# Kernel optimization log

Measured on AMD Instinct MI355X. Metric: run time of the kernel, lower is better.

The kernel has to match this reference:

```python
import jax, jax.numpy as jnp
import numpy as np

POS_W = 1.0
ANG_W = 1.0
WID_W = 1.0
N = 1048560  # predictions (divisible by 17)
M = 8388480  # total GT grasps = sum(arange(N) % 17)


def setup_inputs() -> dict:
    key = jax.random.key(0)
    k1, k2 = jax.random.split(key)
    pred = jax.random.normal(k1, (N, 6), dtype=jnp.float32)
    all_targets = jax.random.normal(k2, (M, 6), dtype=jnp.float32)
    # ragged counts in [0, 16]; sum == M exactly
    target_counts = (jnp.arange(N, dtype=jnp.int64) % 17)
    return {"pred": pred, "all_targets": all_targets, "target_counts": target_counts}


def _smooth_l1(x):
    a = jnp.abs(x)
    return jnp.where(a < 1.0, 0.5 * x * x, a - 0.5)


def reference(pred, all_targets, target_counts):
    n = pred.shape[0]
    m = all_targets.shape[0]
    # segment id for each GT row (contiguous slices, order of target_counts)
    seg = jnp.repeat(jnp.arange(n), target_counts, total_repeat_length=m)  # (M,)
    p = pred[seg]  # (M,6) gathered predictions
    dp = p[:, :2] - all_targets[:, :2]
    da = p[:, 2:4] - all_targets[:, 2:4]
    dw = p[:, 4] - all_targets[:, 4]
    dist = (POS_W * jnp.sum(dp * dp, axis=-1)
            + ANG_W * jnp.sum(da * da, axis=-1)
            + WID_W * dw * dw)  # (M,)
    # ragged argmin per segment (first occurrence, like torch.argmin)
    min_d = jax.ops.segment_min(dist, seg, num_segments=n)  # (N,)
    row = jnp.arange(m)
    cand = jnp.where(dist == min_d[seg], row, m)
    arg = jax.ops.segment_min(cand, seg, num_segments=n)  # (N,) global row idx or m
    has = target_counts > 0
    gt = all_targets[jnp.where(has, jnp.clip(arg, 0, m - 1), 0)]  # (N,6)
    # fused per-prediction loss against the closest GT
    loss_pos = jnp.sum(_smooth_l1(pred[:, :2] - gt[:, :2]), axis=-1)
    loss_ang = jnp.sum(jnp.abs(pred[:, 2:4] - gt[:, 2:4]), axis=-1)
    loss_wid = _smooth_l1(pred[:, 4] - gt[:, 4])
    losses = jnp.where(has, POS_W * loss_pos + ANG_W * loss_ang + WID_W * loss_wid, 0.0)
    return jnp.mean(losses)  # reduction='mean'
```

## Files before the change

### kernel.cpp

```cpp
#include <hip/hip_runtime.h>
#include <math.h>

#define POS_W 1.0f
#define ANG_W 1.0f
#define WID_W 1.0f
#define CHUNK 1024
#define F2PT 12

__device__ __forceinline__ float smooth_l1(float x) {
    float a = fabsf(x);
    return a < 1.0f ? 0.5f * x * x : a - 0.5f;
}

__global__ void k_block_sums(const int* __restrict__ counts, int stride, int n,
                             int* __restrict__ blockSums) {
    int i = blockIdx.x * 256 + threadIdx.x;
    int c = (i < n) ? counts[(long long)i * stride] : 0;
    for (int off = 32; off > 0; off >>= 1) c += __shfl_down(c, off, 64);
    __shared__ int sdata[4];
    int lane = threadIdx.x & 63, wave = threadIdx.x >> 6;
    if (lane == 0) sdata[wave] = c;
    __syncthreads();
    if (threadIdx.x == 0)
        blockSums[blockIdx.x] = sdata[0] + sdata[1] + sdata[2] + sdata[3];
}

__global__ __launch_bounds__(256) void k_loss(
    const float* __restrict__ pred, const float* __restrict__ tgt,
    const int* __restrict__ counts, int stride, int n,
    const int* __restrict__ blockSums, float invN, float* __restrict__ out) {
    __shared__ float2 ch[CHUNK * 3];
    __shared__ int wsum[4];
    __shared__ int wpre[4];
    __shared__ float fs[4];

    int t = threadIdx.x;
    int lane = t & 63, wave = t >> 6;
    int b = blockIdx.x;
    int i = b * 256 + t;
    int c = (i < n) ? counts[(long long)i * stride] : 0;

    int pre = 0;
    for (int j = t; j < b; j += 256) pre += blockSums[j];

    int incl = c;
#pragma unroll
    for (int d = 1; d < 64; d <<= 1) {
        int v = __shfl_up(incl, d, 64);
        if (lane >= d) incl += v;
    }
    for (int o = 32; o > 0; o >>= 1) pre += __shfl_down(pre, o, 64);
    if (lane == 63) wsum[wave] = incl;
    if (lane == 0) wpre[wave] = pre;

    bool active = (i < n) && (c > 0);
    float p0 = 0, p1 = 0, p2 = 0, p3 = 0, p4 = 0;
    if (active) {
        const float2* p2p = (const float2*)(pred + (long long)i * 6);
        float2 a = p2p[0], bb = p2p[1], w = p2p[2];
        p0 = a.x; p1 = a.y; p2 = bb.x; p3 = bb.y; p4 = w.x;
    }

    __syncthreads();
    int w0 = wsum[0], w1 = wsum[1], w2 = wsum[2], w3 = wsum[3];
    int waveOff = (wave > 0 ? w0 : 0) + (wave > 1 ? w1 : 0) + (wave > 2 ? w2 : 0);
    int off = waveOff + incl - c;
    int total = w0 + w1 + w2 + w3;
    int winStart = wpre[0] + wpre[1] + wpre[2] + wpre[3];

    float best = INFINITY;
    float b0 = 0, b1 = 0, b2 = 0, b3 = 0, b4 = 0;

    const float2* win = (const float2*)tgt + (long long)winStart * 3;
    float2 r[F2PT];

    {
        int nF2 = min(CHUNK, total) * 3;
#pragma unroll
        for (int j = 0; j < F2PT; ++j) {
            int k = t + 256 * j;
            if (k < nF2) r[j] = win[k];
        }
    }

    for (int base = 0; base < total; base += CHUNK) {
        int rows = min(CHUNK, total - base);
        int nF2c = rows * 3;
#pragma unroll
        for (int j = 0; j < F2PT; ++j) {
            int k = t + 256 * j;
            if (k < nF2c) ch[k] = r[j];
        }
        __syncthreads();
        int nbase = base + CHUNK;
        if (nbase < total) {
            int nF2n = min(CHUNK, total - nbase) * 3;
            const float2* srcn = win + (long long)nbase * 3;
#pragma unroll
            for (int j = 0; j < F2PT; ++j) {
                int k = t + 256 * j;
                if (k < nF2n) r[j] = srcn[k];
            }
        }
        if (active) {
            int lo = max(off, base), hi = min(off + c, base + rows);
            for (int rr = lo; rr < hi; ++rr) {
                int l3 = (rr - base) * 3;
                float2 ga = ch[l3], gb = ch[l3 + 1], gw = ch[l3 + 2];
                float d0 = p0 - ga.x, d1 = p1 - ga.y;
                float d2 = p2 - gb.x, d3 = p3 - gb.y;
                float d4 = p4 - gw.x;
                float dist = POS_W * (d0 * d0 + d1 * d1) +
                             ANG_W * (d2 * d2 + d3 * d3) + WID_W * d4 * d4;
                if (dist < best) {
                    best = dist;
                    b0 = ga.x; b1 = ga.y; b2 = gb.x; b3 = gb.y; b4 = gw.x;
                }
            }
        }
        __syncthreads();
    }

    float loss = 0.0f;
    if (active) {
        loss = POS_W * (smooth_l1(p0 - b0) + smooth_l1(p1 - b1)) +
               ANG_W * (fabsf(p2 - b2) + fabsf(p3 - b3)) +
               WID_W * smooth_l1(p4 - b4);
    }

    for (int o = 32; o > 0; o >>= 1) loss += __shfl_down(loss, o, 64);
    if (lane == 0) fs[wave] = loss;
    __syncthreads();
    if (t == 0) {
        float tot = (fs[0] + fs[1] + fs[2] + fs[3]) * invN;
        atomicAdd(out, tot);
    }
}

extern "C" void kernel_launch(void* const* d_in, const int* in_sizes, int n_in,
                              void* d_out, int out_size, void* d_ws,
                              size_t ws_size, hipStream_t stream) {
    const float* pred = (const float*)d_in[0];
    const float* tgt = (const float*)d_in[1];
    const int* counts = (const int*)d_in[2];
    int n = in_sizes[0] / 6;
    int stride = (in_sizes[2] == n) ? 1 : 2;
    int nb = (n + 255) / 256;

    int* blockSums = (int*)d_ws;
    float* out = (float*)d_out;

    hipMemsetAsync(d_out, 0, sizeof(float), stream);
    k_block_sums<<<nb, 256, 0, stream>>>(counts, stride, n, blockSums);
    k_loss<<<nb, 256, 0, stream>>>(pred, tgt, counts, stride, n, blockSums,
                                   1.0f / n, out);
}
```

Baseline: 308.0 us.

## Stage target window with aligned float4 loads and lighter LDS barriers

The global-to-LDS staging of the target window now uses 16-byte float4 loads from a window start aligned down to 16 bytes, with a per-block shift that re-indexes rows inside LDS, replacing the 8-byte float2 loads. The block barrier becomes a custom one that waits only on LDS counters, so the register prefetch of the next chunk stays in flight across the barrier. The prefix-sum reads move ahead of the prediction load. The aim is fewer, wider memory instructions and better overlap of loads with compute, at the cost of alignment and bounds arithmetic (an mrows limit) that must be exactly right.

```diff
diff --git a/kernel.cpp b/kernel.cpp
--- a/kernel.cpp
+++ b/kernel.cpp
@@ -1,15 +1,22 @@
 #include <hip/hip_runtime.h>
 #include <math.h>
+#include <stdint.h>
 
 #define POS_W 1.0f
 #define ANG_W 1.0f
 #define WID_W 1.0f
 #define CHUNK 1024
-#define F2PT 12
+#define F4PT 6
 
 __device__ __forceinline__ float smooth_l1(float x) {
     float a = fabsf(x);
     return a < 1.0f ? 0.5f * x * x : a - 0.5f;
+}
+
+__device__ __forceinline__ void bar_lds() {
+    asm volatile("s_waitcnt lgkmcnt(0)" ::: "memory");
+    __builtin_amdgcn_s_barrier();
+    __builtin_amdgcn_sched_barrier(0);
 }
 
 __global__ void k_block_sums(const int* __restrict__ counts, int stride, int n,
@@ -27,9 +34,9 @@
 
 __global__ __launch_bounds__(256) void k_loss(
     const float* __restrict__ pred, const float* __restrict__ tgt,
-    const int* __restrict__ counts, int stride, int n,
+    const int* __restrict__ counts, int stride, int n, int mrows,
     const int* __restrict__ blockSums, float invN, float* __restrict__ out) {
-    __shared__ float2 ch[CHUNK * 3];
+    __shared__ float4 ch4[CHUNK * 3 / 2 + 1];
     __shared__ int wsum[4];
     __shared__ int wpre[4];
     __shared__ float fs[4];
@@ -52,6 +59,13 @@
     for (int o = 32; o > 0; o >>= 1) pre += __shfl_down(pre, o, 64);
     if (lane == 63) wsum[wave] = incl;
     if (lane == 0) wpre[wave] = pre;
+    __syncthreads();
+
+    int w0 = wsum[0], w1 = wsum[1], w2 = wsum[2], w3 = wsum[3];
+    int waveOff = (wave > 0 ? w0 : 0) + (wave > 1 ? w1 : 0) + (wave > 2 ? w2 : 0);
+    int off = waveOff + incl - c;
+    int total = w0 + w1 + w2 + w3;
+    int winStart = wpre[0] + wpre[1] + wpre[2] + wpre[3];
 
     bool active = (i < n) && (c > 0);
     float p0 = 0, p1 = 0, p2 = 0, p3 = 0, p4 = 0;
@@ -61,52 +75,56 @@
         p0 = a.x; p1 = a.y; p2 = bb.x; p3 = bb.y; p4 = w.x;
     }
 
-    __syncthreads();
-    int w0 = wsum[0], w1 = wsum[1], w2 = wsum[2], w3 = wsum[3];
-    int waveOff = (wave > 0 ? w0 : 0) + (wave > 1 ? w1 : 0) + (wave > 2 ? w2 : 0);
-    int off = waveOff + incl - c;
-    int total = w0 + w1 + w2 + w3;
-    int winStart = wpre[0] + wpre[1] + wpre[2] + wpre[3];
+    long long winB = (long long)winStart * 24;
+    long long alignedB = winB & ~15ll;
+    const float4* win4 = (const float4*)((const char*)tgt + alignedB);
+    int sh = (int)(winStart & 1);
+    int f4maxi = (int)(((long long)mrows * 24 - alignedB) >> 4);
 
     float best = INFINITY;
     float b0 = 0, b1 = 0, b2 = 0, b3 = 0, b4 = 0;
-
-    const float2* win = (const float2*)tgt + (long long)winStart * 3;
-    float2 r[F2PT];
+    const float2* ch2 = (const float2*)ch4;
+    float4 rf[F4PT];
 
     {
-        int nF2 = min(CHUNK, total) * 3;
+        int rows0 = min(CHUNK, total);
+        int nF4 = (rows0 * 3 + sh + 1) >> 1;
+        int lim = min(nF4, f4maxi);
 #pragma unroll
-        for (int j = 0; j < F2PT; ++j) {
-            int k = t + 256 * j;
-            if (k < nF2) r[j] = win[k];
+        for (int j = 0; j < F4PT; ++j) {
+            int q = t + 256 * j;
+            if (q < lim) rf[j] = win4[q];
         }
     }
 
     for (int base = 0; base < total; base += CHUNK) {
         int rows = min(CHUNK, total - base);
-        int nF2c = rows * 3;
+        int nF4c = (rows * 3 + sh + 1) >> 1;
+        int qB = (base * 3) >> 1;
+        int lim = min(nF4c, f4maxi - qB);
 #pragma unroll
-        for (int j = 0; j < F2PT; ++j) {
-            int k = t + 256 * j;
-            if (k < nF2c) ch[k] = r[j];
+        for (int j = 0; j < F4PT; ++j) {
+            int q = t + 256 * j;
+            if (q < lim) ch4[q] = rf[j];
         }
-        __syncthreads();
+        bar_lds();
         int nbase = base + CHUNK;
         if (nbase < total) {
-            int nF2n = min(CHUNK, total - nbase) * 3;
-            const float2* srcn = win + (long long)nbase * 3;
+            int rowsn = min(CHUNK, total - nbase);
+            int nF4n = (rowsn * 3 + sh + 1) >> 1;
+            int qBn = (nbase * 3) >> 1;
+            int limn = min(nF4n, f4maxi - qBn);
 #pragma unroll
-            for (int j = 0; j < F2PT; ++j) {
-                int k = t + 256 * j;
-                if (k < nF2n) r[j] = srcn[k];
+            for (int j = 0; j < F4PT; ++j) {
+                int q = t + 256 * j;
+                if (q < limn) rf[j] = win4[qBn + q];
             }
         }
         if (active) {
             int lo = max(off, base), hi = min(off + c, base + rows);
             for (int rr = lo; rr < hi; ++rr) {
-                int l3 = (rr - base) * 3;
-                float2 ga = ch[l3], gb = ch[l3 + 1], gw = ch[l3 + 2];
+                int l2i = (rr - base) * 3 + sh;
+                float2 ga = ch2[l2i], gb = ch2[l2i + 1], gw = ch2[l2i + 2];
                 float d0 = p0 - ga.x, d1 = p1 - ga.y;
                 float d2 = p2 - gb.x, d3 = p3 - gb.y;
                 float d4 = p4 - gw.x;
@@ -118,7 +136,7 @@
                 }
             }
         }
-        __syncthreads();
+        bar_lds();
     }
 
     float loss = 0.0f;
@@ -144,6 +162,7 @@
     const float* tgt = (const float*)d_in[1];
     const int* counts = (const int*)d_in[2];
     int n = in_sizes[0] / 6;
+    int mrows = in_sizes[1] / 6;
     int stride = (in_sizes[2] == n) ? 1 : 2;
     int nb = (n + 255) / 256;
 
@@ -152,6 +171,6 @@
 
     hipMemsetAsync(d_out, 0, sizeof(float), stream);
     k_block_sums<<<nb, 256, 0, stream>>>(counts, stride, n, blockSums);
-    k_loss<<<nb, 256, 0, stream>>>(pred, tgt, counts, stride, n, blockSums,
-                                   1.0f / n, out);
+    k_loss<<<nb, 256, 0, stream>>>(pred, tgt, counts, stride, n, mrows,
+                                   blockSums, 1.0f / n, out);
 }
```

Measured after the change: 361.8 us. 17.5% more time.

## Replace LDS-staged chunk loop with direct per-thread global reads of targets

Applied to the files above, without the earlier changes.

Drops the cooperative block-wide staging of target rows into shared memory, along with its register double-buffering and per-chunk barriers. Each active thread now reads its own contiguous target rows straight from global memory, prefetching one row ahead. This removes the LDS traffic, the synchronisation and the 24 KB LDS footprint, which limited occupancy. In exchange, global loads are no longer coalesced across a wave: each thread walks its own strided segment, relying on caches to absorb the scattered accesses.

```diff
diff --git a/kernel.cpp b/kernel.cpp
--- a/kernel.cpp
+++ b/kernel.cpp
@@ -1,11 +1,10 @@
 #include <hip/hip_runtime.h>
 #include <math.h>
+#include <stdint.h>
 
 #define POS_W 1.0f
 #define ANG_W 1.0f
 #define WID_W 1.0f
-#define CHUNK 1024
-#define F2PT 12
 
 __device__ __forceinline__ float smooth_l1(float x) {
     float a = fabsf(x);
@@ -29,7 +28,6 @@
     const float* __restrict__ pred, const float* __restrict__ tgt,
     const int* __restrict__ counts, int stride, int n,
     const int* __restrict__ blockSums, float invN, float* __restrict__ out) {
-    __shared__ float2 ch[CHUNK * 3];
     __shared__ int wsum[4];
     __shared__ int wpre[4];
     __shared__ float fs[4];
@@ -60,65 +58,37 @@
         float2 a = p2p[0], bb = p2p[1], w = p2p[2];
         p0 = a.x; p1 = a.y; p2 = bb.x; p3 = bb.y; p4 = w.x;
     }
+    __syncthreads();
 
-    __syncthreads();
     int w0 = wsum[0], w1 = wsum[1], w2 = wsum[2], w3 = wsum[3];
     int waveOff = (wave > 0 ? w0 : 0) + (wave > 1 ? w1 : 0) + (wave > 2 ? w2 : 0);
     int off = waveOff + incl - c;
-    int total = w0 + w1 + w2 + w3;
     int winStart = wpre[0] + wpre[1] + wpre[2] + wpre[3];
 
     float best = INFINITY;
     float b0 = 0, b1 = 0, b2 = 0, b3 = 0, b4 = 0;
 
-    const float2* win = (const float2*)tgt + (long long)winStart * 3;
-    float2 r[F2PT];
-
-    {
-        int nF2 = min(CHUNK, total) * 3;
-#pragma unroll
-        for (int j = 0; j < F2PT; ++j) {
-            int k = t + 256 * j;
-            if (k < nF2) r[j] = win[k];
+    if (active) {
+        const float2* rp =
+            (const float2*)tgt + (long long)(winStart + off) * 3;
+        float2 ga = rp[0], gb = rp[1], gw = rp[2];
+        for (int rr = 0; rr < c; ++rr) {
+            float2 na, nb, nw;
+            if (rr + 1 < c) {
+                int q = (rr + 1) * 3;
+                na = rp[q]; nb = rp[q + 1]; nw = rp[q + 2];
+            }
+            float d0 = p0 - ga.x, d1 = p1 - ga.y;
+            float d2 = p2 - gb.x, d3 = p3 - gb.y;
+            float d4 = p4 - gw.x;
+            float dist = POS_W * (d0 * d0 + d1 * d1) +
+                         ANG_W * (d2 * d2 + d3 * d3) + WID_W * d4 * d4;
+            if (dist < best) {
+                best = dist;
+                b0 = ga.x; b1 = ga.y; b2 = gb.x; b3 = gb.y; b4 = gw.x;
+            }
+            ga = na; gb = nb; gw = nw;
         }
-    }
-
-    for (int base = 0; base < total; base += CHUNK) {
-        int rows = min(CHUNK, total - base);
-        int nF2c = rows * 3;
-#pragma unroll
-        for (int j = 0; j < F2PT; ++j) {
-            int k = t + 256 * j;
-            if (k < nF2c) ch[k] = r[j];
-        }
-        __syncthreads();
-        int nbase = base + CHUNK;
-        if (nbase < total) {
-            int nF2n = min(CHUNK, total - nbase) * 3;
-            const float2* srcn = win + (long long)nbase * 3;
-#pragma unroll
-            for (int j = 0; j < F2PT; ++j) {
-                int k = t + 256 * j;
-                if (k < nF2n) r[j] = srcn[k];
-            }
-        }
-        if (active) {
-            int lo = max(off, base), hi = min(off + c, base + rows);
-            for (int rr = lo; rr < hi; ++rr) {
-                int l3 = (rr - base) * 3;
-                float2 ga = ch[l3], gb = ch[l3 + 1], gw = ch[l3 + 2];
-                float d0 = p0 - ga.x, d1 = p1 - ga.y;
-                float d2 = p2 - gb.x, d3 = p3 - gb.y;
-                float d4 = p4 - gw.x;
-                float dist = POS_W * (d0 * d0 + d1 * d1) +
-                             ANG_W * (d2 * d2 + d3 * d3) + WID_W * d4 * d4;
-                if (dist < best) {
-                    best = dist;
-                    b0 = ga.x; b1 = ga.y; b2 = gb.x; b3 = gb.y; b4 = gw.x;
-                }
-            }
-        }
-        __syncthreads();
     }
 
     float loss = 0.0f;
```

Result: slower. 342.5 us (+11.2%).
